# Kernel tuning notes

Measured on AMD Instinct MI355X. Metric: run time of the kernel, lower is better.

## Reference

```python
import jax, jax.numpy as jnp
import numpy as np

D_MODEL = 2560
NUM_HEADS = 32
NUM_KV_HEADS = 8
HEAD_DIM = 128
ROPE_THETA = 5e6
EPS = 1e-6
G = NUM_KV_HEADS
Q_PER_KV = NUM_HEADS // NUM_KV_HEADS


def setup_inputs() -> dict:
    key = jax.random.key(0)
    ks = jax.random.split(key, 5)
    B, S = 1, 2048
    scale = 0.02
    return {
        "x": jax.random.normal(ks[0], (B, S, D_MODEL), jnp.float32),
        "Wq": jax.random.normal(ks[1], (NUM_HEADS * HEAD_DIM, D_MODEL), jnp.float32) * scale,
        "Wk": jax.random.normal(ks[2], (NUM_KV_HEADS * HEAD_DIM, D_MODEL), jnp.float32) * scale,
        "Wv": jax.random.normal(ks[3], (NUM_KV_HEADS * HEAD_DIM, D_MODEL), jnp.float32) * scale,
        "Wo": jax.random.normal(ks[4], (D_MODEL, NUM_HEADS * HEAD_DIM), jnp.float32) * scale,
        "q_norm_w": jnp.ones((HEAD_DIM,), jnp.float32),
        "k_norm_w": jnp.ones((HEAD_DIM,), jnp.float32),
    }


def _rms_norm(x, w):
    var = jnp.mean(jnp.square(x), axis=-1, keepdims=True)
    return x * jax.lax.rsqrt(var + EPS) * w


def _rope(x, pos):
    # x: (b, h, s, d); HF-style rotate_half RoPE
    d = x.shape[-1]
    inv_freq = 1.0 / (ROPE_THETA ** (jnp.arange(0, d, 2, dtype=jnp.float32) / d))
    ang = pos[:, None].astype(jnp.float32) * inv_freq[None, :]      # (s, d/2)
    cos = jnp.concatenate([jnp.cos(ang), jnp.cos(ang)], axis=-1)     # (s, d)
    sin = jnp.concatenate([jnp.sin(ang), jnp.sin(ang)], axis=-1)
    x1, x2 = x[..., : d // 2], x[..., d // 2 :]
    rot = jnp.concatenate([-x2, x1], axis=-1)
    return x * cos + rot * sin


def reference(x, Wq, Wk, Wv, Wo, q_norm_w, k_norm_w):
    B, S, _ = x.shape
    pos = jnp.arange(S)
    q = (x @ Wq.T).reshape(B, S, NUM_HEADS, HEAD_DIM).transpose(0, 2, 1, 3)
    k = (x @ Wk.T).reshape(B, S, NUM_KV_HEADS, HEAD_DIM).transpose(0, 2, 1, 3)
    v = (x @ Wv.T).reshape(B, S, NUM_KV_HEADS, HEAD_DIM).transpose(0, 2, 1, 3)
    q = _rope(_rms_norm(q, q_norm_w), pos)
    k = _rope(_rms_norm(k, k_norm_w), pos)
    new_cache_k, new_cache_v = k, v
    # GQA: (b, g, h, s, d) against (b, g, k, d)
    qg = q.reshape(B, G, Q_PER_KV, S, HEAD_DIM)
    scores = jnp.einsum("bghsd,bgkd->bghsk", qg, k) / (HEAD_DIM ** 0.5)
    causal = jnp.triu(jnp.full((S, S), -jnp.inf, jnp.float32), k=1)
    scores = scores + causal
    attn = jax.nn.softmax(scores, axis=-1)
    out = jnp.einsum("bghsk,bgkd->bghsd", attn, v)
    out = out.reshape(B, NUM_HEADS, S, HEAD_DIM).transpose(0, 2, 1, 3).reshape(B, S, NUM_HEADS * HEAD_DIM)
    out = out @ Wo.T
    return (out, new_cache_k, new_cache_v)
```

## Files before the change

kernel.cpp:

```cpp
#include <hip/hip_runtime.h>
#include <hip/hip_bf16.h>
#include <math.h>

#define S_LEN  2048
#define DMODEL 2560
#define NHEADS 32
#define NKV    8
#define HD     128
#define QKDIM  (NHEADS * HD)
#define KVDIM  (NKV * HD)

typedef __bf16 bf16x8 __attribute__((ext_vector_type(8)));
typedef float  f32x4  __attribute__((ext_vector_type(4)));
typedef unsigned short u16;

#define AS1 __attribute__((address_space(1)))
#define AS3 __attribute__((address_space(3)))

__device__ __forceinline__ void load16_to_lds(const void* g, void* l) {
    __builtin_amdgcn_global_load_lds((const AS1 void*)g, (AS3 void*)l, 16, 0, 0);
}

__device__ __forceinline__ u16 f2bf(float f) {
    unsigned u = __builtin_bit_cast(unsigned, f);
    return (u16)((u + 0x7fff + ((u >> 16) & 1)) >> 16);
}

#define PHASE_BAR() do { __builtin_amdgcn_sched_barrier(0);            \
                         __builtin_amdgcn_s_barrier();                 \
                         __builtin_amdgcn_sched_barrier(0); } while (0)
#define WAIT_LGKM0() do { asm volatile("s_waitcnt lgkmcnt(0)" ::: "memory"); \
                          __builtin_amdgcn_sched_barrier(0); } while (0)

__device__ __forceinline__ const bf16x8* fragp(const __bf16* hbase, int row, int colb) {
    int b = (row << 7) | colb;
    b ^= ((b >> 7) & 7) << 4;
    return (const bf16x8*)((const char*)hbase + b);
}

__device__ __forceinline__ void stage_half(const __bf16* __restrict__ g0, int Kp,
                                           __bf16* l0, int wave, int lane) {
#pragma unroll
    for (int j = 0; j < 2; ++j) {
        const int p = ((wave * 2 + j) << 10) | (lane << 4);
        const int b = p ^ (((p >> 7) & 7) << 4);
        load16_to_lds((const char*)g0 + (size_t)(b >> 7) * (Kp * 2) + (b & 127),
                      (char*)l0 + ((wave * 2 + j) << 10));
    }
}

#define N4_X   (S_LEN * DMODEL / 4)
#define N4_WQ  (QKDIM * DMODEL / 4)
#define N4_WK  (KVDIM * DMODEL / 4)
#define N4_ALL (N4_X + N4_WQ + 2 * N4_WK)

__global__ __launch_bounds__(256) void convert_inputs(const float* __restrict__ x,
                                                      const float* __restrict__ wq,
                                                      const float* __restrict__ wk,
                                                      const float* __restrict__ wv,
                                                      u16* __restrict__ xb,
                                                      u16* __restrict__ wb) {
    const int stride = gridDim.x * 256;
    for (int i = blockIdx.x * 256 + threadIdx.x; i < N4_ALL; i += stride) {
        const float4* src;
        ushort4* dst;
        if (i < N4_X) {
            src = (const float4*)x + i;
            dst = (ushort4*)xb + i;
        } else {
            const int j = i - N4_X;
            dst = (ushort4*)wb + j;
            if (j < N4_WQ)                  src = (const float4*)wq + j;
            else if (j < N4_WQ + N4_WK)     src = (const float4*)wk + (j - N4_WQ);
            else                            src = (const float4*)wv + (j - N4_WQ - N4_WK);
        }
        float4 v = *src;
        ushort4 r;
        r.x = f2bf(v.x); r.y = f2bf(v.y); r.z = f2bf(v.z); r.w = f2bf(v.w);
        *dst = r;
    }
}

__global__ __launch_bounds__(256) void f32_to_bf16_k(const float* __restrict__ in,
                                                     u16* __restrict__ out, int n4) {
    int i = blockIdx.x * 256 + threadIdx.x;
    const int stride = gridDim.x * 256;
    for (; i < n4; i += stride) {
        float4 v = ((const float4*)in)[i];
        ushort4 r;
        r.x = f2bf(v.x); r.y = f2bf(v.y); r.z = f2bf(v.z); r.w = f2bf(v.w);
        ((ushort4*)out)[i] = r;
    }
}

__global__ __launch_bounds__(64) void rope_table(float* __restrict__ ct,
                                                 float* __restrict__ st) {
    const int s = blockIdx.x;
    const int i = threadIdx.x;
    const double invf = pow(5.0e6, -(double)i / 64.0);
    const double ang  = (double)s * invf;
    ct[s * 64 + i] = (float)cos(ang);
    st[s * 64 + i] = (float)sin(ang);
}

__global__ __launch_bounds__(256) void gemm_bf16_nt(const __bf16* __restrict__ A,
                                                    const __bf16* __restrict__ B,
                                                    float* __restrict__ C,
                                                    int M, int N, int K) {
    __shared__ __align__(16) __bf16 Als[128 * 64];
    __shared__ __align__(16) __bf16 Bls[128 * 64];
    const int tid  = threadIdx.x;
    const int lane = tid & 63;
    const int wave = tid >> 6;
    const int wm   = wave >> 1, wn = wave & 1;
    const int m0   = blockIdx.y * 128;
    const int n0   = blockIdx.x * 128;
    const int frow = lane & 15;
    const int fkq  = lane >> 4;

    f32x4 acc[4][4];
#pragma unroll
    for (int t = 0; t < 4; ++t)
#pragma unroll
        for (int u = 0; u < 4; ++u)
            acc[t][u] = (f32x4){0.f, 0.f, 0.f, 0.f};

    for (int k0 = 0; k0 < K; k0 += 64) {
        __syncthreads();
#pragma unroll
        for (int i = 0; i < 2; ++i) {
            const int mt  = i * 4 + wave;
            const int row = mt * 16 + frow;
#pragma unroll
            for (int kh = 0; kh < 2; ++kh) {
                const int col = k0 + kh * 32 + fkq * 8;
                load16_to_lds(A + (size_t)(m0 + row) * K + col,
                              &Als[(size_t)((mt * 2 + kh) * 64) * 8]);
                load16_to_lds(B + (size_t)(n0 + row) * K + col,
                              &Bls[(size_t)((mt * 2 + kh) * 64) * 8]);
            }
        }
        __syncthreads();

#pragma unroll
        for (int kh = 0; kh < 2; ++kh) {
            bf16x8 af[4], bfr[4];
#pragma unroll
            for (int t = 0; t < 4; ++t)
                af[t]  = *(const bf16x8*)&Als[(((wm * 4 + t) * 2 + kh) * 64 + lane) * 8];
#pragma unroll
            for (int u = 0; u < 4; ++u)
                bfr[u] = *(const bf16x8*)&Bls[(((wn * 4 + u) * 2 + kh) * 64 + lane) * 8];
#pragma unroll
            for (int t = 0; t < 4; ++t)
#pragma unroll
                for (int u = 0; u < 4; ++u)
                    acc[t][u] = __builtin_amdgcn_mfma_f32_16x16x32_bf16(
                                    af[t], bfr[u], acc[t][u], 0, 0, 0);
        }
    }

    const int crow = (lane >> 4) * 4;
    const int ccol = lane & 15;
#pragma unroll
    for (int t = 0; t < 4; ++t) {
        const int gr = m0 + (wm * 4 + t) * 16 + crow;
#pragma unroll
        for (int u = 0; u < 4; ++u) {
            const int gc = n0 + (wn * 4 + u) * 16 + ccol;
#pragma unroll
            for (int r = 0; r < 4; ++r)
                C[(size_t)(gr + r) * N + gc] = acc[t][u][r];
        }
    }
}

__global__ __launch_bounds__(512, 2) void gemm_qkv_8ph(const __bf16* __restrict__ A,
                                                       const __bf16* __restrict__ Bq,
                                                       const __bf16* __restrict__ Bkv,
                                                       const float* __restrict__ ct,
                                                       const float* __restrict__ st,
                                                       const float* __restrict__ qw,
                                                       const float* __restrict__ kw,
                                                       u16*   __restrict__ qrb,
                                                       float* __restrict__ kc,
                                                       u16*   __restrict__ kcb,
                                                       float* __restrict__ vc,
                                                       u16*   __restrict__ vtb) {
    __shared__ __align__(16) __bf16 Als[4][128 * 64];
    __shared__ __align__(16) __bf16 Bls[4][128 * 64];

    const int K   = DMODEL;
    const int nkt = K / 64;
    const int n0g = blockIdx.x * 256;
    const __bf16* B;
    int n0;
    if (n0g < QKDIM) { B = Bq;  n0 = n0g; }
    else             { B = Bkv; n0 = n0g - QKDIM; }
    const int m0 = blockIdx.y * 256;

    const int tid  = threadIdx.x;
    const int lane = tid & 63;
    const int wave = tid >> 6;
    const int wm   = wave >> 1;
    const int wn   = wave & 1;
    const int frow = lane & 15;
    const int fkq  = lane >> 4;
    const int ha   = wm >> 1;
    const int ar0  = (wm & 1) * 64 + frow;

    f32x4 acc[4][8];
#pragma unroll
    for (int t = 0; t < 4; ++t)
#pragma unroll
        for (int u = 0; u < 8; ++u)
            acc[t][u] = (f32x4){0.f, 0.f, 0.f, 0.f};

    stage_half(A + (size_t)m0 * K,               K, Als[0], wave, lane);
    stage_half(A + (size_t)(m0 + 128) * K,       K, Als[1], wave, lane);
    stage_half(B + (size_t)n0 * K,               K, Bls[0], wave, lane);
    stage_half(B + (size_t)(n0 + 128) * K,       K, Bls[1], wave, lane);
    stage_half(A + (size_t)m0 * K + 64,          K, Als[2], wave, lane);
    stage_half(B + (size_t)n0 * K + 64,          K, Bls[2], wave, lane);
    stage_half(B + (size_t)(n0 + 128) * K + 64,  K, Bls[3], wave, lane);
    asm volatile("s_waitcnt vmcnt(6)" ::: "memory");
    PHASE_BAR();

    for (int kt = 0; kt < nkt; ++kt) {
        const int bf = kt & 1;
        const __bf16* Ahb = Als[bf * 2 + ha];
        const __bf16* Bhb = Bls[bf * 2 + wn];

        bf16x8 a0[2][2], b0[4][2];
#pragma unroll
        for (int mt = 0; mt < 2; ++mt)
#pragma unroll
            for (int kh = 0; kh < 2; ++kh)
                a0[mt][kh] = *fragp(Ahb, ar0 + mt * 16, kh * 64 + fkq * 16);
#pragma unroll
        for (int nt = 0; nt < 4; ++nt)
#pragma unroll
            for (int kh = 0; kh < 2; ++kh)
                b0[nt][kh] = *fragp(Bhb, nt * 16 + frow, kh * 64 + fkq * 16);
        if (kt + 1 < nkt)
            stage_half(A + (size_t)(m0 + 128) * K + (kt + 1) * 64, K,
                       Als[(bf ^ 1) * 2 + 1], wave, lane);
        asm volatile("s_waitcnt lgkmcnt(8)" ::: "memory");
        PHASE_BAR();
        WAIT_LGKM0();
        __builtin_amdgcn_s_setprio(1);
#pragma unroll
        for (int mt = 0; mt < 2; ++mt)
#pragma unroll
            for (int nt = 0; nt < 4; ++nt)
#pragma unroll
                for (int kh = 0; kh < 2; ++kh)
                    acc[mt][nt] = __builtin_amdgcn_mfma_f32_16x16x32_bf16(
                                      a0[mt][kh], b0[nt][kh], acc[mt][nt], 0, 0, 0);
        __builtin_amdgcn_s_setprio(0);
        PHASE_BAR();

        bf16x8 a1[2][2];
#pragma unroll
        for (int mt = 0; mt < 2; ++mt)
#pragma unroll
            for (int kh = 0; kh < 2; ++kh)
                a1[mt][kh] = *fragp(Ahb, ar0 + 32 + mt * 16, kh * 64 + fkq * 16);
        PHASE_BAR();
        WAIT_LGKM0();
        __builtin_amdgcn_s_setprio(1);
#pragma unroll
        for (int mt = 0; mt < 2; ++mt)
#pragma unroll
            for (int nt = 0; nt < 4; ++nt)
#pragma unroll
                for (int kh = 0; kh < 2; ++kh)
                    acc[2 + mt][nt] = __builtin_amdgcn_mfma_f32_16x16x32_bf16(
                                          a1[mt][kh], b0[nt][kh], acc[2 + mt][nt], 0, 0, 0);
        __builtin_amdgcn_s_setprio(0);
        PHASE_BAR();

        bf16x8 b1[4][2];
#pragma unroll
        for (int nt = 0; nt < 4; ++nt)
#pragma unroll
            for (int kh = 0; kh < 2; ++kh)
                b1[nt][kh] = *fragp(Bhb, (4 + nt) * 16 + frow, kh * 64 + fkq * 16);
        if (kt + 2 < nkt)
            stage_half(A + (size_t)m0 * K + (kt + 2) * 64, K,
                       Als[bf * 2 + 0], wave, lane);
        PHASE_BAR();
        WAIT_LGKM0();
        __builtin_amdgcn_s_setprio(1);
#pragma unroll
        for (int mt = 0; mt < 2; ++mt)
#pragma unroll
            for (int nt = 0; nt < 4; ++nt)
#pragma unroll
                for (int kh = 0; kh < 2; ++kh)
                    acc[2 + mt][4 + nt] = __builtin_amdgcn_mfma_f32_16x16x32_bf16(
                                              a1[mt][kh], b1[nt][kh], acc[2 + mt][4 + nt], 0, 0, 0);
        __builtin_amdgcn_s_setprio(0);
        PHASE_BAR();

        if (kt + 2 < nkt) {
            stage_half(B + (size_t)n0 * K + (kt + 2) * 64,         K,
                       Bls[bf * 2 + 0], wave, lane);
            stage_half(B + (size_t)(n0 + 128) * K + (kt + 2) * 64, K,
                       Bls[bf * 2 + 1], wave, lane);
        }
        PHASE_BAR();
        WAIT_LGKM0();
        __builtin_amdgcn_s_setprio(1);
#pragma unroll
        for (int mt = 0; mt < 2; ++mt)
#pragma unroll
            for (int nt = 0; nt < 4; ++nt)
#pragma unroll
                for (int kh = 0; kh < 2; ++kh)
                    acc[mt][4 + nt] = __builtin_amdgcn_mfma_f32_16x16x32_bf16(
                                          a0[mt][kh], b1[nt][kh], acc[mt][4 + nt], 0, 0, 0);
        __builtin_amdgcn_s_setprio(0);
        if (kt < nkt - 2) asm volatile("s_waitcnt vmcnt(6)" ::: "memory");
        else              asm volatile("s_waitcnt vmcnt(0)" ::: "memory");
        PHASE_BAR();
    }

    const int fr = frow;
    const int fq = fkq;
    const int nw = n0g + wn * 128;
    if (n0g < QKDIM + KVDIM) {
        const int isQ = (n0g < QKDIM) ? 1 : 0;
        const float* w = isQ ? qw : kw;
        float wv[8];
#pragma unroll
        for (int u = 0; u < 8; ++u) wv[u] = w[u * 16 + fr];

#pragma unroll
        for (int mt = 0; mt < 4; ++mt) {
#pragma unroll
            for (int r = 0; r < 4; ++r) {
                float ss = 0.f;
#pragma unroll
                for (int u = 0; u < 8; ++u) ss += acc[mt][u][r] * acc[mt][u][r];
                ss += __shfl_xor(ss, 1);
                ss += __shfl_xor(ss, 2);
                ss += __shfl_xor(ss, 4);
                ss += __shfl_xor(ss, 8);
                const float rstd = rsqrtf(ss * (1.0f / 128.0f) + 1e-6f);
                const int s = m0 + wm * 64 + mt * 16 + fq * 4 + r;
#pragma unroll
                for (int u = 0; u < 4; ++u) {
                    const float cs  = ct[s * 64 + u * 16 + fr];
                    const float sn  = st[s * 64 + u * 16 + fr];
                    const float ylo = acc[mt][u][r]     * rstd * wv[u];
                    const float yhi = acc[mt][u + 4][r] * rstd * wv[u + 4];
                    const float olo = ylo * cs - yhi * sn;
                    const float ohi = yhi * cs + ylo * sn;
                    if (isQ) {
                        const int h = nw >> 7;
                        const size_t base = ((size_t)h * S_LEN + s) * HD;
                        qrb[base + u * 16 + fr]       = f2bf(olo * 0.12751743f);
                        qrb[base + (u + 4) * 16 + fr] = f2bf(ohi * 0.12751743f);
                    } else {
                        const int g = (nw - QKDIM) >> 7;
                        const size_t base = ((size_t)g * S_LEN + s) * HD;
                        kc [base + u * 16 + fr]       = olo;
                        kc [base + (u + 4) * 16 + fr] = ohi;
                        kcb[base + u * 16 + fr]       = f2bf(olo);
                        kcb[base + (u + 4) * 16 + fr] = f2bf(ohi);
                    }
                }
            }
        }
    } else {
        const int g = (nw - QKDIM - KVDIM) >> 7;
#pragma unroll
        for (int mt = 0; mt < 4; ++mt) {
            const int sb = m0 + wm * 64 + mt * 16 + fq * 4;
#pragma unroll
            for (int u = 0; u < 8; ++u) {
                const int d = u * 16 + fr;
                ushort4 o;
                o.x = f2bf(acc[mt][u][0]); o.y = f2bf(acc[mt][u][1]);
                o.z = f2bf(acc[mt][u][2]); o.w = f2bf(acc[mt][u][3]);
                *(ushort4*)&vtb[((size_t)g * HD + d) * S_LEN + sb] = o;
#pragma unroll
                for (int r = 0; r < 4; ++r)
                    vc[((size_t)g * S_LEN + sb + r) * HD + d] = acc[mt][u][r];
            }
        }
    }
}

__device__ __forceinline__ void attn_tile_swapped(
        const bf16x8 aq[4], f32x4 o_acc[8], float& m_i, float& l_i,
        const __bf16* __restrict__ Kl, const __bf16* __restrict__ Vl,
        int lane, int fr, int fq, int qm, int kbase, bool diag) {
    f32x4 sT[4];
#pragma unroll
    for (int u = 0; u < 4; ++u) sT[u] = (f32x4){0.f, 0.f, 0.f, 0.f};
    __builtin_amdgcn_s_setprio(1);
#pragma unroll
    for (int u = 0; u < 4; ++u)
#pragma unroll
        for (int ks = 0; ks < 4; ++ks)
            sT[u] = __builtin_amdgcn_mfma_f32_16x16x32_bf16(
                        *(const bf16x8*)&Kl[((u * 4 + ks) * 64 + lane) * 8],
                        aq[ks], sT[u], 0, 0, 0);
    __builtin_amdgcn_s_setprio(0);

    if (diag) {
#pragma unroll
        for (int u = 0; u < 4; ++u)
#pragma unroll
            for (int r = 0; r < 4; ++r)
                if (kbase + u * 16 + fq * 4 + r > qm + fr)
                    sT[u][r] = -INFINITY;
    }

    float mx = sT[0][0];
#pragma unroll
    for (int u = 0; u < 4; ++u)
#pragma unroll
        for (int r = 0; r < 4; ++r) mx = fmaxf(mx, sT[u][r]);
    mx = fmaxf(mx, __shfl_xor(mx, 16));
    mx = fmaxf(mx, __shfl_xor(mx, 32));

    if (__any(mx > m_i + 8.0f)) {
        const float m_new = fmaxf(m_i, mx);
        const float alpha = exp2f(m_i - m_new);
        m_i = m_new;
        l_i *= alpha;
#pragma unroll
        for (int r = 0; r < 4; ++r) {
            const float a = __shfl(alpha, fq * 4 + r);
#pragma unroll
            for (int dt = 0; dt < 8; ++dt) o_acc[dt][r] *= a;
        }
    }

    float p[4][4];
    float ps = 0.f;
#pragma unroll
    for (int u = 0; u < 4; ++u)
#pragma unroll
        for (int r = 0; r < 4; ++r) {
            p[u][r] = exp2f(sT[u][r] - m_i);
            ps += p[u][r];
        }
    ps += __shfl_xor(ps, 16);
    ps += __shfl_xor(ps, 32);
    l_i += ps;

    unsigned pk[4][2];
#pragma unroll
    for (int u = 0; u < 4; ++u)
#pragma unroll
        for (int hh = 0; hh < 2; ++hh)
            asm("v_cvt_pk_bf16_f32 %0, %1, %2"
                : "=v"(pk[u][hh]) : "v"(p[u][2 * hh]), "v"(p[u][2 * hh + 1]));

    const int slA = fr + 16 * ((fq & 1) * 2);
    const int slB = slA + 16;
    bf16x8 ap[2];
#pragma unroll
    for (int ks = 0; ks < 2; ++ks) {
        unsigned w[4];
#pragma unroll
        for (int jp = 0; jp < 4; ++jp) {
            const int sl = (jp & 2) ? slB : slA;
            const unsigned v0 = (unsigned)__shfl((int)pk[2 * ks + 0][jp & 1], sl);
            const unsigned v1 = (unsigned)__shfl((int)pk[2 * ks + 1][jp & 1], sl);
            w[jp] = (fq & 2) ? v1 : v0;
        }
        ap[ks] = __builtin_bit_cast(bf16x8, (uint4){w[0], w[1], w[2], w[3]});
    }

    __builtin_amdgcn_s_setprio(1);
#pragma unroll
    for (int dt = 0; dt < 8; ++dt)
#pragma unroll
        for (int ks = 0; ks < 2; ++ks)
            o_acc[dt] = __builtin_amdgcn_mfma_f32_16x16x32_bf16(
                            ap[ks],
                            *(const bf16x8*)&Vl[((dt * 2 + ks) * 64 + lane) * 8],
                            o_acc[dt], 0, 0, 0);
    __builtin_amdgcn_s_setprio(0);
}

__global__ __launch_bounds__(256, 2) void attn_mfma(const __bf16* __restrict__ Qb,
                                                    const __bf16* __restrict__ Kb,
                                                    const __bf16* __restrict__ Vt,
                                                    u16* __restrict__ Ob) {
    __shared__ __align__(16) __bf16 Kls[2][16 * 64 * 8];
    __shared__ __align__(16) __bf16 Vls[2][16 * 64 * 8];

    const int h    = blockIdx.x;
    const int g    = h >> 2;
    const int pair = blockIdx.y;
    const int ytl  = pair;
    const int yth  = (S_LEN / 64 - 1) - pair;
    const int q0l  = ytl * 64;
    const int q0h  = yth * 64;
    const int tid  = threadIdx.x;
    const int lane = tid & 63;
    const int wave = tid >> 6;
    const int fr   = lane & 15;
    const int fq   = lane >> 4;

    {
        const __bf16* Qh = Qb + ((size_t)h * S_LEN + q0h + wave * 16 + fr) * HD;
        const __bf16* Ql = Qb + ((size_t)h * S_LEN + q0l + wave * 16 + fr) * HD;
#pragma unroll
        for (int ks = 0; ks < 4; ++ks) {
            load16_to_lds(Qh + ks * 32 + fq * 8, &Kls[0][(size_t)((wave * 4 + ks) * 64) * 8]);
            load16_to_lds(Ql + ks * 32 + fq * 8, &Kls[1][(size_t)((wave * 4 + ks) * 64) * 8]);
        }
    }
    __syncthreads();
    bf16x8 aqh[4], aql[4];
#pragma unroll
    for (int ks = 0; ks < 4; ++ks) {
        aqh[ks] = *(const bf16x8*)&Kls[0][((wave * 4 + ks) * 64 + lane) * 8];
        aql[ks] = *(const bf16x8*)&Kls[1][((wave * 4 + ks) * 64 + lane) * 8];
    }
    __syncthreads();

    float m_h = -INFINITY, l_h = 0.f, m_l = -INFINITY, l_l = 0.f;
    f32x4 o_h[8], o_l[8];
#pragma unroll
    for (int dt = 0; dt < 8; ++dt) {
        o_h[dt] = (f32x4){0.f, 0.f, 0.f, 0.f};
        o_l[dt] = (f32x4){0.f, 0.f, 0.f, 0.f};
    }

    {
        const __bf16* Kg = Kb + ((size_t)g * S_LEN + wave * 16 + fr) * HD;
#pragma unroll
        for (int ks = 0; ks < 4; ++ks)
            load16_to_lds(Kg + ks * 32 + fq * 8, &Kls[0][(size_t)((wave * 4 + ks) * 64) * 8]);
#pragma unroll
        for (int i = 0; i < 2; ++i) {
            const int dt = wave * 2 + i;
            const __bf16* Vg = Vt + ((size_t)g * HD + dt * 16 + fr) * S_LEN;
#pragma unroll
            for (int ks = 0; ks < 2; ++ks)
                load16_to_lds(Vg + ks * 32 + fq * 8, &Vls[0][(size_t)((dt * 2 + ks) * 64) * 8]);
        }
    }
    __syncthreads();

    for (int kt = 0; kt <= yth; ++kt) {
        const int buf = kt & 1;
        if (kt < yth) {
            const int nb = buf ^ 1;
            const __bf16* Kg = Kb + ((size_t)g * S_LEN + (kt + 1) * 64 + wave * 16 + fr) * HD;
#pragma unroll
            for (int ks = 0; ks < 4; ++ks)
                load16_to_lds(Kg + ks * 32 + fq * 8, &Kls[nb][(size_t)((wave * 4 + ks) * 64) * 8]);
#pragma unroll
            for (int i = 0; i < 2; ++i) {
                const int dt = wave * 2 + i;
                const __bf16* Vg = Vt + ((size_t)g * HD + dt * 16 + fr) * S_LEN + (kt + 1) * 64;
#pragma unroll
                for (int ks = 0; ks < 2; ++ks)
                    load16_to_lds(Vg + ks * 32 + fq * 8, &Vls[nb][(size_t)((dt * 2 + ks) * 64) * 8]);
            }
        }

        attn_tile_swapped(aqh, o_h, m_h, l_h, Kls[buf], Vls[buf],
                          lane, fr, fq, q0h + wave * 16, kt * 64, kt == yth);
        if (kt <= ytl)
            attn_tile_swapped(aql, o_l, m_l, l_l, Kls[buf], Vls[buf],
                              lane, fr, fq, q0l + wave * 16, kt * 64, kt == ytl);

        __syncthreads();
    }

#pragma unroll
    for (int r = 0; r < 4; ++r) {
        const float ih = 1.0f / __shfl(l_h, fq * 4 + r);
        const float il = 1.0f / __shfl(l_l, fq * 4 + r);
        const int sh = q0h + wave * 16 + fq * 4 + r;
        const int sl = q0l + wave * 16 + fq * 4 + r;
#pragma unroll
        for (int dt = 0; dt < 8; ++dt) {
            Ob[(size_t)sh * QKDIM + h * HD + dt * 16 + fr] = f2bf(o_h[dt][r] * ih);
            Ob[(size_t)sl * QKDIM + h * HD + dt * 16 + fr] = f2bf(o_l[dt][r] * il);
        }
    }
}

extern "C" void kernel_launch(void* const* d_in, const int* in_sizes, int n_in,
                              void* d_out, int out_size, void* d_ws, size_t ws_size,
                              hipStream_t stream) {
    const float* x  = (const float*)d_in[0];
    const float* Wq = (const float*)d_in[1];
    const float* Wk = (const float*)d_in[2];
    const float* Wv = (const float*)d_in[3];
    const float* Wo = (const float*)d_in[4];
    const float* qw = (const float*)d_in[5];
    const float* kw = (const float*)d_in[6];

    float* out     = (float*)d_out;
    float* cache_k = out + (size_t)S_LEN * DMODEL;
    float* cache_v = cache_k + (size_t)NKV * S_LEN * HD;

    u16* wsu = (u16*)d_ws;
    u16* qrb = wsu;
    u16* kcb = qrb + (size_t)NHEADS * S_LEN * HD;
    u16* vtb = kcb + (size_t)NKV * S_LEN * HD;
    u16* Wqb = vtb + (size_t)NKV * S_LEN * HD;
    u16* Wkb = Wqb + (size_t)QKDIM * DMODEL;
    u16* aob = Wqb;
    u16* Wob = aob + (size_t)S_LEN * QKDIM;
    float* ct = (float*)(Wqb + (size_t)S_LEN * QKDIM + (size_t)DMODEL * QKDIM);
    float* st = ct + S_LEN * 64;
    u16* xb  = (u16*)out;

    convert_inputs<<<4096, 256, 0, stream>>>(x, Wq, Wk, Wv, xb, Wqb);
    rope_table<<<S_LEN, 64, 0, stream>>>(ct, st);

    gemm_qkv_8ph<<<dim3((QKDIM + 2 * KVDIM) / 256, S_LEN / 256), 512, 0, stream>>>(
        (const __bf16*)xb, (const __bf16*)Wqb, (const __bf16*)Wkb,
        ct, st, qw, kw, qrb, cache_k, kcb, cache_v, vtb);

    f32_to_bf16_k<<<1024, 256, 0, stream>>>(Wo, Wob, DMODEL * QKDIM / 4);
    attn_mfma<<<dim3(NHEADS, S_LEN / 128), 256, 0, stream>>>(
        (const __bf16*)qrb, (const __bf16*)kcb, (const __bf16*)vtb, aob);

    gemm_bf16_nt<<<dim3(DMODEL / 128, S_LEN / 128), 256, 0, stream>>>(
        (const __bf16*)aob, (const __bf16*)Wob, out, S_LEN, DMODEL, QKDIM);
}
```

Measured before the change: 455.0 us.

## Replace output projection GEMM with pipelined 256x256 split-K kernel using atomics

The simple 128x128 output projection GEMM is replaced by an 8-phase software-pipelined 256x256-tile kernel that reuses the QKV GEMM's staging helpers. K is split three ways across blockIdx.z (22/21/21 steps of 64) and results are accumulated into the output with float atomics. The output is zeroed inside a combined Wo-conversion prep kernel. This aims to raise MFMA utilisation and keep enough blocks in flight for a 10x8 tile grid, at the cost of atomic traffic and nondeterministic summation order.

Measured after the change: 422.7 us. -7.1%, faster.

```diff
diff --git a/kernel.cpp b/kernel.cpp
--- a/kernel.cpp
+++ b/kernel.cpp
@@ -81,15 +81,23 @@
     }
 }
 
-__global__ __launch_bounds__(256) void f32_to_bf16_k(const float* __restrict__ in,
-                                                     u16* __restrict__ out, int n4) {
-    int i = blockIdx.x * 256 + threadIdx.x;
+#define N4_OUT (S_LEN * DMODEL / 4)
+#define N4_WO  (DMODEL * QKDIM / 4)
+
+__global__ __launch_bounds__(256) void prep_outproj(const float* __restrict__ wo,
+                                                    u16* __restrict__ wob,
+                                                    float* __restrict__ outz) {
     const int stride = gridDim.x * 256;
-    for (; i < n4; i += stride) {
-        float4 v = ((const float4*)in)[i];
-        ushort4 r;
-        r.x = f2bf(v.x); r.y = f2bf(v.y); r.z = f2bf(v.z); r.w = f2bf(v.w);
-        ((ushort4*)out)[i] = r;
+    for (int i = blockIdx.x * 256 + threadIdx.x; i < N4_OUT + N4_WO; i += stride) {
+        if (i < N4_OUT) {
+            ((float4*)outz)[i] = (float4){0.f, 0.f, 0.f, 0.f};
+        } else {
+            const int j = i - N4_OUT;
+            float4 v = ((const float4*)wo)[j];
+            ushort4 r;
+            r.x = f2bf(v.x); r.y = f2bf(v.y); r.z = f2bf(v.z); r.w = f2bf(v.w);
+            ((ushort4*)wob)[j] = r;
+        }
     }
 }
 
@@ -101,78 +109,6 @@
     const double ang  = (double)s * invf;
     ct[s * 64 + i] = (float)cos(ang);
     st[s * 64 + i] = (float)sin(ang);
-}
-
-__global__ __launch_bounds__(256) void gemm_bf16_nt(const __bf16* __restrict__ A,
-                                                    const __bf16* __restrict__ B,
-                                                    float* __restrict__ C,
-                                                    int M, int N, int K) {
-    __shared__ __align__(16) __bf16 Als[128 * 64];
-    __shared__ __align__(16) __bf16 Bls[128 * 64];
-    const int tid  = threadIdx.x;
-    const int lane = tid & 63;
-    const int wave = tid >> 6;
-    const int wm   = wave >> 1, wn = wave & 1;
-    const int m0   = blockIdx.y * 128;
-    const int n0   = blockIdx.x * 128;
-    const int frow = lane & 15;
-    const int fkq  = lane >> 4;
-
-    f32x4 acc[4][4];
-#pragma unroll
-    for (int t = 0; t < 4; ++t)
-#pragma unroll
-        for (int u = 0; u < 4; ++u)
-            acc[t][u] = (f32x4){0.f, 0.f, 0.f, 0.f};
-
-    for (int k0 = 0; k0 < K; k0 += 64) {
-        __syncthreads();
-#pragma unroll
-        for (int i = 0; i < 2; ++i) {
-            const int mt  = i * 4 + wave;
-            const int row = mt * 16 + frow;
-#pragma unroll
-            for (int kh = 0; kh < 2; ++kh) {
-                const int col = k0 + kh * 32 + fkq * 8;
-                load16_to_lds(A + (size_t)(m0 + row) * K + col,
-                              &Als[(size_t)((mt * 2 + kh) * 64) * 8]);
-                load16_to_lds(B + (size_t)(n0 + row) * K + col,
-                              &Bls[(size_t)((mt * 2 + kh) * 64) * 8]);
-            }
-        }
-        __syncthreads();
-
-#pragma unroll
-        for (int kh = 0; kh < 2; ++kh) {
-            bf16x8 af[4], bfr[4];
-#pragma unroll
-            for (int t = 0; t < 4; ++t)
-                af[t]  = *(const bf16x8*)&Als[(((wm * 4 + t) * 2 + kh) * 64 + lane) * 8];
-#pragma unroll
-            for (int u = 0; u < 4; ++u)
-                bfr[u] = *(const bf16x8*)&Bls[(((wn * 4 + u) * 2 + kh) * 64 + lane) * 8];
-#pragma unroll
-            for (int t = 0; t < 4; ++t)
-#pragma unroll
-                for (int u = 0; u < 4; ++u)
-                    acc[t][u] = __builtin_amdgcn_mfma_f32_16x16x32_bf16(
-                                    af[t], bfr[u], acc[t][u], 0, 0, 0);
-        }
-    }
-
-    const int crow = (lane >> 4) * 4;
-    const int ccol = lane & 15;
-#pragma unroll
-    for (int t = 0; t < 4; ++t) {
-        const int gr = m0 + (wm * 4 + t) * 16 + crow;
-#pragma unroll
-        for (int u = 0; u < 4; ++u) {
-            const int gc = n0 + (wn * 4 + u) * 16 + ccol;
-#pragma unroll
-            for (int r = 0; r < 4; ++r)
-                C[(size_t)(gr + r) * N + gc] = acc[t][u][r];
-        }
-    }
 }
 
 __global__ __launch_bounds__(512, 2) void gemm_qkv_8ph(const __bf16* __restrict__ A,
@@ -393,6 +329,160 @@
     }
 }
 
+__global__ __launch_bounds__(512, 2) void gemm_out_8ph(const __bf16* __restrict__ A,
+                                                       const __bf16* __restrict__ B,
+                                                       float* __restrict__ C) {
+    __shared__ __align__(16) __bf16 Als[4][128 * 64];
+    __shared__ __align__(16) __bf16 Bls[4][128 * 64];
+
+    const int K   = QKDIM;
+    const int z   = blockIdx.z;
+    const int ks0 = (z == 0) ? 0 : 22 + (z - 1) * 21;
+    const int L   = (z == 0) ? 22 : 21;
+    const int ko0 = ks0 * 64;
+    const int n0  = blockIdx.x * 256;
+    const int m0  = blockIdx.y * 256;
+
+    const int tid  = threadIdx.x;
+    const int lane = tid & 63;
+    const int wave = tid >> 6;
+    const int wm   = wave >> 1;
+    const int wn   = wave & 1;
+    const int frow = lane & 15;
+    const int fkq  = lane >> 4;
+    const int ha   = wm >> 1;
+    const int ar0  = (wm & 1) * 64 + frow;
+
+    f32x4 acc[4][8];
+#pragma unroll
+    for (int t = 0; t < 4; ++t)
+#pragma unroll
+        for (int u = 0; u < 8; ++u)
+            acc[t][u] = (f32x4){0.f, 0.f, 0.f, 0.f};
+
+    stage_half(A + (size_t)m0 * K + ko0,              K, Als[0], wave, lane);
+    stage_half(A + (size_t)(m0 + 128) * K + ko0,      K, Als[1], wave, lane);
+    stage_half(B + (size_t)n0 * K + ko0,              K, Bls[0], wave, lane);
+    stage_half(B + (size_t)(n0 + 128) * K + ko0,      K, Bls[1], wave, lane);
+    stage_half(A + (size_t)m0 * K + ko0 + 64,         K, Als[2], wave, lane);
+    stage_half(B + (size_t)n0 * K + ko0 + 64,         K, Bls[2], wave, lane);
+    stage_half(B + (size_t)(n0 + 128) * K + ko0 + 64, K, Bls[3], wave, lane);
+    asm volatile("s_waitcnt vmcnt(6)" ::: "memory");
+    PHASE_BAR();
+
+    for (int j = 0; j < L; ++j) {
+        const int bf = j & 1;
+        const __bf16* Ahb = Als[bf * 2 + ha];
+        const __bf16* Bhb = Bls[bf * 2 + wn];
+
+        bf16x8 a0[2][2], b0[4][2];
+#pragma unroll
+        for (int mt = 0; mt < 2; ++mt)
+#pragma unroll
+            for (int kh = 0; kh < 2; ++kh)
+                a0[mt][kh] = *fragp(Ahb, ar0 + mt * 16, kh * 64 + fkq * 16);
+#pragma unroll
+        for (int nt = 0; nt < 4; ++nt)
+#pragma unroll
+            for (int kh = 0; kh < 2; ++kh)
+                b0[nt][kh] = *fragp(Bhb, nt * 16 + frow, kh * 64 + fkq * 16);
+        if (j + 1 < L)
+            stage_half(A + (size_t)(m0 + 128) * K + ko0 + (j + 1) * 64, K,
+                       Als[(bf ^ 1) * 2 + 1], wave, lane);
+        asm volatile("s_waitcnt lgkmcnt(8)" ::: "memory");
+        PHASE_BAR();
+        WAIT_LGKM0();
+        __builtin_amdgcn_s_setprio(1);
+#pragma unroll
+        for (int mt = 0; mt < 2; ++mt)
+#pragma unroll
+            for (int nt = 0; nt < 4; ++nt)
+#pragma unroll
+                for (int kh = 0; kh < 2; ++kh)
+                    acc[mt][nt] = __builtin_amdgcn_mfma_f32_16x16x32_bf16(
+                                      a0[mt][kh], b0[nt][kh], acc[mt][nt], 0, 0, 0);
+        __builtin_amdgcn_s_setprio(0);
+        PHASE_BAR();
+
+        bf16x8 a1[2][2];
+#pragma unroll
+        for (int mt = 0; mt < 2; ++mt)
+#pragma unroll
+            for (int kh = 0; kh < 2; ++kh)
+                a1[mt][kh] = *fragp(Ahb, ar0 + 32 + mt * 16, kh * 64 + fkq * 16);
+        PHASE_BAR();
+        WAIT_LGKM0();
+        __builtin_amdgcn_s_setprio(1);
+#pragma unroll
+        for (int mt = 0; mt < 2; ++mt)
+#pragma unroll
+            for (int nt = 0; nt < 4; ++nt)
+#pragma unroll
+                for (int kh = 0; kh < 2; ++kh)
+                    acc[2 + mt][nt] = __builtin_amdgcn_mfma_f32_16x16x32_bf16(
+                                          a1[mt][kh], b0[nt][kh], acc[2 + mt][nt], 0, 0, 0);
+        __builtin_amdgcn_s_setprio(0);
+        PHASE_BAR();
+
+        bf16x8 b1[4][2];
+#pragma unroll
+        for (int nt = 0; nt < 4; ++nt)
+#pragma unroll
+            for (int kh = 0; kh < 2; ++kh)
+                b1[nt][kh] = *fragp(Bhb, (4 + nt) * 16 + frow, kh * 64 + fkq * 16);
+        if (j + 2 < L)
+            stage_half(A + (size_t)m0 * K + ko0 + (j + 2) * 64, K,
+                       Als[bf * 2 + 0], wave, lane);
+        PHASE_BAR();
+        WAIT_LGKM0();
+        __builtin_amdgcn_s_setprio(1);
+#pragma unroll
+        for (int mt = 0; mt < 2; ++mt)
+#pragma unroll
+            for (int nt = 0; nt < 4; ++nt)
+#pragma unroll
+                for (int kh = 0; kh < 2; ++kh)
+                    acc[2 + mt][4 + nt] = __builtin_amdgcn_mfma_f32_16x16x32_bf16(
+                                              a1[mt][kh], b1[nt][kh], acc[2 + mt][4 + nt], 0, 0, 0);
+        __builtin_amdgcn_s_setprio(0);
+        PHASE_BAR();
+
+        if (j + 2 < L) {
+            stage_half(B + (size_t)n0 * K + ko0 + (j + 2) * 64,         K,
+                       Bls[bf * 2 + 0], wave, lane);
+            stage_half(B + (size_t)(n0 + 128) * K + ko0 + (j + 2) * 64, K,
+                       Bls[bf * 2 + 1], wave, lane);
+        }
+        PHASE_BAR();
+        WAIT_LGKM0();
+        __builtin_amdgcn_s_setprio(1);
+#pragma unroll
+        for (int mt = 0; mt < 2; ++mt)
+#pragma unroll
+            for (int nt = 0; nt < 4; ++nt)
+#pragma unroll
+                for (int kh = 0; kh < 2; ++kh)
+                    acc[mt][4 + nt] = __builtin_amdgcn_mfma_f32_16x16x32_bf16(
+                                          a0[mt][kh], b1[nt][kh], acc[mt][4 + nt], 0, 0, 0);
+        __builtin_amdgcn_s_setprio(0);
+        if (j < L - 2) asm volatile("s_waitcnt vmcnt(6)" ::: "memory");
+        else           asm volatile("s_waitcnt vmcnt(0)" ::: "memory");
+        PHASE_BAR();
+    }
+
+#pragma unroll
+    for (int mt = 0; mt < 4; ++mt) {
+#pragma unroll
+        for (int r = 0; r < 4; ++r) {
+            const int s = m0 + wm * 64 + mt * 16 + fkq * 4 + r;
+            float* crow = C + (size_t)s * DMODEL + n0 + wn * 128 + frow;
+#pragma unroll
+            for (int u = 0; u < 8; ++u)
+                unsafeAtomicAdd(crow + u * 16, acc[mt][u][r]);
+        }
+    }
+}
+
 __device__ __forceinline__ void attn_tile_swapped(
         const bf16x8 aq[4], f32x4 o_acc[8], float& m_i, float& l_i,
         const __bf16* __restrict__ Kl, const __bf16* __restrict__ Vl,
@@ -626,10 +716,10 @@
         (const __bf16*)xb, (const __bf16*)Wqb, (const __bf16*)Wkb,
         ct, st, qw, kw, qrb, cache_k, kcb, cache_v, vtb);
 
-    f32_to_bf16_k<<<1024, 256, 0, stream>>>(Wo, Wob, DMODEL * QKDIM / 4);
+    prep_outproj<<<2048, 256, 0, stream>>>(Wo, Wob, out);
     attn_mfma<<<dim3(NHEADS, S_LEN / 128), 256, 0, stream>>>(
         (const __bf16*)qrb, (const __bf16*)kcb, (const __bf16*)vtb, aob);
 
-    gemm_bf16_nt<<<dim3(DMODEL / 128, S_LEN / 128), 256, 0, stream>>>(
-        (const __bf16*)aob, (const __bf16*)Wob, out, S_LEN, DMODEL, QKDIM);
-}
+    gemm_out_8ph<<<dim3(DMODEL / 256, S_LEN / 256, 3), 512, 0, stream>>>(
+        (const __bf16*)aob, (const __bf16*)Wob, out);
+}
```
